# Kernel tuning notes

Hardware: AMD Instinct MI355X
Metric: run time of the kernel (lower is better)

The kernel has to match this reference:

```python
import jax, jax.numpy as jnp
import numpy as np

B, DIM, H = 65536, 1024, 16
HD = DIM // H  # head dim = 64


def setup_inputs() -> dict:
    key = jax.random.key(0)
    ks = jax.random.split(key, 6)
    x = jax.random.normal(ks[0], (B, DIM), dtype=jnp.float32)
    y = jax.random.normal(ks[1], (B, DIM), dtype=jnp.float32)
    mask = jnp.zeros((B,), dtype=jnp.bool_)  # unused by the module
    # Parameters (qkv_bias=False -> no bias on q/kv; proj has bias)
    Wq = jax.random.normal(ks[2], (DIM, DIM), dtype=jnp.float32) * 0.02
    Wkv = jax.random.normal(ks[3], (DIM, 2 * DIM), dtype=jnp.float32) * 0.02
    Wproj = jax.random.normal(ks[4], (DIM, DIM), dtype=jnp.float32) * 0.02
    bproj = jax.random.normal(ks[5], (DIM,), dtype=jnp.float32) * 0.02
    return {"x": x, "y": y, "mask": mask, "Wq": Wq, "Wkv": Wkv,
            "Wproj": Wproj, "bproj": bproj}


def reference(x, y, mask, Wq, Wkv, Wproj, bproj):
    # mask is accepted but unused, matching the original module.
    scale = HD ** (-0.5)
    q = x @ Wq                      # [B, DIM]
    kv = y @ Wkv                    # [B, 2*DIM]
    k, v = jnp.split(kv, 2, axis=-1)
    # b (h d) -> b h d
    q = q.reshape(B, H, HD) * scale  # first scale (q *= scale)
    k = k.reshape(B, H, HD)
    v = v.reshape(B, H, HD)
    # per-head dot product, scaled AGAIN (faithful to original double-scale)
    dots = jnp.einsum("bhd,bhd->bh", q, k) * scale  # [B, H]
    attn = jax.nn.softmax(dots, axis=-1)             # softmax over heads
    out = attn[..., None] * v                        # [B, H, HD]
    out = out.reshape(B, DIM)                        # b h d -> b (h d)
    return out @ Wproj + bproj
```

## Files before the change

kernel.cpp:

```cpp
#include <hip/hip_runtime.h>

typedef unsigned short ushort_t;
typedef unsigned int   uint_t;

typedef ushort_t u16x8  __attribute__((ext_vector_type(8)));
typedef __bf16   bf16x8 __attribute__((ext_vector_type(8)));
typedef float    f32x4  __attribute__((ext_vector_type(4)));

#define DIMSZ 1024

__device__ __forceinline__ ushort_t f2bf(float f) {
  uint_t u = __builtin_bit_cast(uint_t, f);
  u += 0x7fffu + ((u >> 16) & 1u);
  return (ushort_t)(u >> 16);
}
__device__ __forceinline__ float bf2f(ushort_t h) {
  uint_t u = ((uint_t)h) << 16;
  return __builtin_bit_cast(float, u);
}
__device__ __forceinline__ void lds_load16(const void* g, void* l) {
  __builtin_amdgcn_global_load_lds((const __attribute__((address_space(1))) void*)g,
                                   (__attribute__((address_space(3))) void*)l, 16, 0, 0);
}
#define SCHED0() __builtin_amdgcn_sched_barrier(0)
#define WBAR() do { SCHED0(); __builtin_amdgcn_s_barrier(); SCHED0(); } while (0)

__global__ __launch_bounds__(256) void wtrans(const float* __restrict__ src, int ld,
                                              ushort_t* __restrict__ dst) {
  __shared__ ushort_t tile[32][33];
  const int bx = blockIdx.x, by = blockIdx.y;
  const int tx = threadIdx.x & 31, ty = threadIdx.x >> 5;
#pragma unroll
  for (int i = 0; i < 32; i += 8)
    tile[ty + i][tx] = f2bf(src[(size_t)(by * 32 + ty + i) * ld + bx * 32 + tx]);
  __syncthreads();
#pragma unroll
  for (int i = 0; i < 32; i += 8)
    dst[(size_t)(bx * 32 + ty + i) * 1024 + by * 32 + tx] = tile[tx][ty + i];
}

__global__ __launch_bounds__(256) void cvt_bf16(const float* __restrict__ s,
                                                ushort_t* __restrict__ d) {
  const size_t n8 = (size_t)65536 * 1024 / 8;
  const size_t stride = (size_t)gridDim.x * 256;
  for (size_t i = (size_t)blockIdx.x * 256 + threadIdx.x; i < n8; i += stride) {
    f32x4 f0 = *(const f32x4*)(s + i * 8);
    f32x4 f1 = *(const f32x4*)(s + i * 8 + 4);
    u16x8 o;
#pragma unroll
    for (int j = 0; j < 4; ++j) { o[j] = f2bf(f0[j]); o[4 + j] = f2bf(f1[j]); }
    *(u16x8*)(d + i * 8) = o;
  }
}

__global__ __launch_bounds__(256) void softmax16(float* __restrict__ d) {
  const int row = blockIdx.x * 256 + threadIdx.x;
  f32x4 v[4];
#pragma unroll
  for (int i = 0; i < 4; ++i) v[i] = *(const f32x4*)(d + (size_t)row * 16 + i * 4);
  float m = v[0][0];
#pragma unroll
  for (int i = 0; i < 4; ++i)
#pragma unroll
    for (int j = 0; j < 4; ++j) m = fmaxf(m, v[i][j]);
  float sum = 0.f;
#pragma unroll
  for (int i = 0; i < 4; ++i)
#pragma unroll
    for (int j = 0; j < 4; ++j) { v[i][j] = expf(v[i][j] - m); sum += v[i][j]; }
  const float r = 1.f / sum;
#pragma unroll
  for (int i = 0; i < 4; ++i) {
#pragma unroll
    for (int j = 0; j < 4; ++j) v[i][j] *= r;
    *(f32x4*)(d + (size_t)row * 16 + i * 4) = v[i];
  }
}

__global__ __launch_bounds__(256) void abk(const ushort_t* __restrict__ kvb,
                                           const float* __restrict__ at,
                                           ushort_t* __restrict__ ab) {
  const size_t stride = (size_t)gridDim.x * 256;
  for (size_t g = (size_t)blockIdx.x * 256 + threadIdx.x; g < (size_t)8388608; g += stride) {
    const int row = (int)(g >> 7), c8 = (int)(g & 127);
    const float sc = at[(size_t)row * 16 + (c8 >> 3)];
    u16x8 v8 = *(const u16x8*)(kvb + (size_t)row * 2048 + 1024 + c8 * 8);
    u16x8 o;
#pragma unroll
    for (int j = 0; j < 8; ++j) o[j] = f2bf(bf2f(v8[j]) * sc);
    *(u16x8*)(ab + (size_t)row * 1024 + c8 * 8) = o;
  }
}

template <int EPI>
__global__ __launch_bounds__(512, 2) void gemm8(const ushort_t* __restrict__ A,
                                                const ushort_t* __restrict__ Bt,
                                                void* __restrict__ Cv,
                                                const float* __restrict__ bias,
                                                const ushort_t* __restrict__ kvp,
                                                float* __restrict__ dots,
                                                int ldc, int ncol_lg2) {
  __shared__ ushort_t lds[65536];
  const int t = threadIdx.x;
  const int nb8 = gridDim.x >> 3;
  const int nbid = (blockIdx.x & 7) * nb8 + (blockIdx.x >> 3);
  const int n0 = (nbid & ((1 << ncol_lg2) - 1)) * 256;
  const int m0 = (nbid >> ncol_lg2) * 256;
  const int w = t >> 6, lane = t & 63;
  const int wm = w >> 2, wn = w & 3;
  const int lr = lane & 15, lk = lane >> 4;
  const int w512 = w * 512;

  const int srow = w * 8 + (lane >> 3);
  const int scsw = ((lane & 7) * 16) ^ ((srow & 7) << 4);
  const ushort_t* aS = A + (size_t)(m0 + srow) * DIMSZ + (scsw >> 1);
  const ushort_t* bS = Bt + (size_t)(n0 + srow) * DIMSZ + (scsw >> 1);

  const int cbe0 = (((lk * 16)) ^ ((lr & 7) << 4)) >> 1;
  const int cbe1 = ((64 + lk * 16) ^ ((lr & 7) << 4)) >> 1;
  const int aRB = lr * 64;
  const int bRB = 32768 + (wn * 64 + lr) * 64;

  f32x4 acc[8][4];
  const f32x4 zf = {0.f, 0.f, 0.f, 0.f};
#pragma unroll
  for (int i = 0; i < 8; ++i)
#pragma unroll
    for (int j = 0; j < 4; ++j) acc[i][j] = zf;
  bf16x8 a[4][2], b0[2][2], b1[2][2];

#define STAGE_A(cc, hh, tt) do {                                          \
    const ushort_t* s_ = aS + (size_t)(hh) * 65536 + (tt) * 64;           \
    ushort_t* d_ = lds + (cc) * 16384 + (hh) * 4096 + w512;               \
    lds_load16(s_, d_);                                                   \
    lds_load16(s_ + 131072, d_ + 8192); } while (0)
#define STAGE_B(cc, hh, tt) do {                                          \
    const ushort_t* s_ = bS + (size_t)(hh) * 131072 + (tt) * 64;          \
    ushort_t* d_ = lds + 32768 + (cc) * 16384 + (hh) * 8192 + w512;       \
    lds_load16(s_, d_);                                                   \
    lds_load16(s_ + 65536, d_ + 4096); } while (0)
#define LDA(cc, mq) do {                                                  \
    const ushort_t* Lp = lds + (cc) * 16384 + (wm * 2 + (mq)) * 4096 + aRB; \
    _Pragma("unroll") for (int j = 0; j < 4; ++j) {                       \
      a[j][0] = *(const bf16x8*)(Lp + j * 1024 + cbe0);                   \
      a[j][1] = *(const bf16x8*)(Lp + j * 1024 + cbe1); } } while (0)
#define LDB(cc, dst, nq) do {                                             \
    const ushort_t* Lp = lds + (cc) * 16384 + bRB + (nq) * 2048;          \
    _Pragma("unroll") for (int ni = 0; ni < 2; ++ni) {                    \
      dst[ni][0] = *(const bf16x8*)(Lp + ni * 1024 + cbe0);               \
      dst[ni][1] = *(const bf16x8*)(Lp + ni * 1024 + cbe1); } } while (0)
#define MMQ(mb, B, nb) do {                                               \
    _Pragma("unroll") for (int j = 0; j < 4; ++j)                         \
    _Pragma("unroll") for (int ni = 0; ni < 2; ++ni)                      \
    _Pragma("unroll") for (int ks = 0; ks < 2; ++ks)                      \
      acc[(mb) + j][(nb) + ni] = __builtin_amdgcn_mfma_f32_16x16x32_bf16( \
          a[j][ks], B[ni][ks], acc[(mb) + j][(nb) + ni], 0, 0, 0); } while (0)
#define TILE(S1, S2, VM, tv, c, nxt) do {                                 \
    LDA(c, 0); LDB(c, b0, 0);                                             \
    if (S1) STAGE_A(nxt, 1, (tv) + 1);                                    \
    WBAR();                                                               \
    __builtin_amdgcn_s_setprio(1); MMQ(0, b0, 0); __builtin_amdgcn_s_setprio(0); \
    WBAR();                                                               \
    LDB(c, b1, 1);                                                        \
    if (S2) STAGE_A(c, 0, (tv) + 2);                                      \
    WBAR();                                                               \
    __builtin_amdgcn_s_setprio(1); MMQ(0, b1, 2); __builtin_amdgcn_s_setprio(0); \
    WBAR();                                                               \
    LDA(c, 1);                                                            \
    if (S2) STAGE_B(c, 0, (tv) + 2);                                      \
    WBAR();                                                               \
    __builtin_amdgcn_s_setprio(1); MMQ(4, b1, 2); __builtin_amdgcn_s_setprio(0); \
    WBAR();                                                               \
    if (S2) STAGE_B(c, 1, (tv) + 2);                                      \
    if ((VM) == 6) { asm volatile("s_waitcnt vmcnt(6)" ::: "memory"); }   \
    else if ((VM) == 0) { asm volatile("s_waitcnt vmcnt(0)" ::: "memory"); } \
    WBAR();                                                               \
    __builtin_amdgcn_s_setprio(1); MMQ(4, b0, 0); __builtin_amdgcn_s_setprio(0); \
    WBAR();                                                               \
  } while (0)

  STAGE_A(0, 0, 0); STAGE_A(0, 1, 0); STAGE_B(0, 0, 0); STAGE_B(0, 1, 0);
  STAGE_A(1, 0, 1); STAGE_B(1, 0, 1); STAGE_B(1, 1, 1);
  asm volatile("s_waitcnt vmcnt(6)" ::: "memory");
  WBAR();

  for (int tt = 0; tt < 7; ++tt) {
    const int t0 = tt * 2;
    TILE(1, 1, 6, t0, 0, 1);
    TILE(1, 1, 6, t0 + 1, 1, 0);
  }
  TILE(1, 0, 0, 14, 0, 1);
  TILE(0, 0, -1, 15, 1, 0);

#undef TILE
#undef MMQ
#undef LDB
#undef LDA
#undef STAGE_B
#undef STAGE_A

  if constexpr (EPI == 0) {
    ushort_t* Cp = (ushort_t*)Cv;
    ushort_t* ep = lds + w * 8192;
#pragma unroll
    for (int mq = 0; mq < 2; ++mq)
#pragma unroll
      for (int j = 0; j < 4; ++j)
#pragma unroll
        for (int ni = 0; ni < 4; ++ni)
#pragma unroll
          for (int r = 0; r < 4; ++r) {
            const int row = mq * 64 + j * 16 + lk * 4 + r;
            const int ce = ((ni * 16 + lr) * 2) ^ ((row & 7) << 4);
            ep[row * 64 + (ce >> 1)] = f2bf(acc[mq * 4 + j][ni][r]);
          }
#pragma unroll
    for (int rr = 0; rr < 16; ++rr) {
      const int row = rr * 8 + (lane >> 3);
      const int ce = ((lane & 7) * 16) ^ ((lane >> 3) << 4);
      u16x8 vv = *(const u16x8*)(ep + row * 64 + (ce >> 1));
      *(u16x8*)(Cp + (size_t)(m0 + wm * 128 + row) * ldc + n0 + wn * 64 + (lane & 7) * 8) = vv;
    }
  } else if constexpr (EPI == 1) {
    float* Op = (float*)Cv;
    float bb[4];
#pragma unroll
    for (int ni = 0; ni < 4; ++ni) bb[ni] = bias[n0 + wn * 64 + ni * 16 + lr];
#pragma unroll
    for (int mq = 0; mq < 2; ++mq)
#pragma unroll
      for (int j = 0; j < 4; ++j)
#pragma unroll
        for (int ni = 0; ni < 4; ++ni)
#pragma unroll
          for (int r = 0; r < 4; ++r)
            Op[(size_t)(m0 + wm * 128 + mq * 64 + j * 16 + lk * 4 + r) * 1024 +
               n0 + wn * 64 + ni * 16 + lr] = acc[mq * 4 + j][ni][r] + bb[ni];
  } else {
    const int h = (n0 >> 6) + wn;
    ushort_t* kw = lds + w * 8192;
    const int rsub = lane >> 3, c8 = (lane & 7) * 8;
    const ushort_t* kS = kvp + (size_t)(m0 + wm * 128 + rsub) * 2048 + h * 64 + c8;
#pragma unroll
    for (int i = 0; i < 16; ++i)
      lds_load16(kS + (size_t)i * 8 * 2048, kw + i * 512);
    asm volatile("s_waitcnt vmcnt(0)" ::: "memory");
#pragma unroll
    for (int mq = 0; mq < 2; ++mq)
#pragma unroll
      for (int j = 0; j < 4; ++j)
#pragma unroll
        for (int r = 0; r < 4; ++r) {
          const int row = mq * 64 + j * 16 + lk * 4 + r;
          float p = 0.f;
#pragma unroll
          for (int ni = 0; ni < 4; ++ni)
            p += acc[mq * 4 + j][ni][r] * bf2f(kw[row * 64 + ni * 16 + lr]);
#pragma unroll
          for (int off = 1; off < 16; off <<= 1) p += __shfl_xor(p, off, 16);
          if (lr == 0)
            dots[(size_t)(m0 + wm * 128 + row) * 16 + h] = p * 0.015625f;
        }
  }
}

extern "C" void kernel_launch(void* const* d_in, const int* in_sizes, int n_in,
                              void* d_out, int out_size, void* d_ws, size_t ws_size,
                              hipStream_t stream) {
  const float* x   = (const float*)d_in[0];
  const float* y   = (const float*)d_in[1];
  const float* Wq  = (const float*)d_in[3];
  const float* Wkv = (const float*)d_in[4];
  const float* Wp  = (const float*)d_in[5];
  const float* bp  = (const float*)d_in[6];
  (void)in_sizes; (void)n_in; (void)out_size; (void)ws_size;

  char* ws = (char*)d_ws;
  ushort_t* Wqt   = (ushort_t*)(ws);
  ushort_t* Wkvt  = (ushort_t*)(ws + (2ull   << 20));
  ushort_t* Wpt   = (ushort_t*)(ws + (6ull   << 20));
  float*    dotsb = (float*)   (ws + (8ull   << 20));
  ushort_t* kvb   = (ushort_t*)(ws + (12ull  << 20));
  ushort_t* actb  = (ushort_t*)(ws + (268ull << 20));

  wtrans<<<dim3(32, 32), 256, 0, stream>>>(Wq, 1024, Wqt);
  wtrans<<<dim3(64, 32), 256, 0, stream>>>(Wkv, 2048, Wkvt);
  wtrans<<<dim3(32, 32), 256, 0, stream>>>(Wp, 1024, Wpt);

  cvt_bf16<<<4096, 256, 0, stream>>>(y, actb);
  gemm8<0><<<2048, 512, 0, stream>>>(actb, Wkvt, kvb, nullptr, nullptr, nullptr, 2048, 3);

  cvt_bf16<<<4096, 256, 0, stream>>>(x, actb);
  gemm8<2><<<1024, 512, 0, stream>>>(actb, Wqt, nullptr, nullptr, kvb, dotsb, 1024, 2);

  softmax16<<<256, 256, 0, stream>>>(dotsb);

  abk<<<2048, 256, 0, stream>>>(kvb, dotsb, actb);

  gemm8<1><<<1024, 512, 0, stream>>>(actb, Wpt, d_out, bp, nullptr, nullptr, 1024, 2);
}
```

Before: 813.6 us.

## Simplify GEMM main loop to whole-tile double buffering with fewer barriers

Replaces the fine-grained 8-wave ping-pong schedule, which staged quarter tiles between MMA phases and had eight barriers per tile, with a simpler loop. Each iteration now loads all B fragments and the A fragments, runs all MFMAs, then issues the full next-next tile load behind a single barrier pair. The LDS layout becomes two contiguous 256x64 A|B buffers. This cuts barrier and scheduling overhead but gives up the fine interleaving of global-to-LDS loads with compute, and keeps more B fragments live in registers.

```diff
diff --git a/kernel.cpp b/kernel.cpp
--- a/kernel.cpp
+++ b/kernel.cpp
@@ -109,17 +109,16 @@
   const int w = t >> 6, lane = t & 63;
   const int wm = w >> 2, wn = w & 3;
   const int lr = lane & 15, lk = lane >> 4;
-  const int w512 = w * 512;
-
-  const int srow = w * 8 + (lane >> 3);
-  const int scsw = ((lane & 7) * 16) ^ ((srow & 7) << 4);
-  const ushort_t* aS = A + (size_t)(m0 + srow) * DIMSZ + (scsw >> 1);
-  const ushort_t* bS = Bt + (size_t)(n0 + srow) * DIMSZ + (scsw >> 1);
-
-  const int cbe0 = (((lk * 16)) ^ ((lr & 7) << 4)) >> 1;
+
+  const int sr = lane >> 3;
+  const int scsw = ((lane & 7) * 16) ^ ((sr & 7) << 4);
+  const ushort_t* aS = A + (size_t)(m0 + w * 8 + sr) * DIMSZ + (scsw >> 1);
+  const ushort_t* bS = Bt + (size_t)(n0 + w * 8 + sr) * DIMSZ + (scsw >> 1);
+
+  const int cbe0 = ((lk * 16) ^ ((lr & 7) << 4)) >> 1;
   const int cbe1 = ((64 + lk * 16) ^ ((lr & 7) << 4)) >> 1;
-  const int aRB = lr * 64;
-  const int bRB = 32768 + (wn * 64 + lr) * 64;
+  const int aRowB = (wm * 128 + lr) * 64;
+  const int bRowB = 16384 + (wn * 64 + lr) * 64;
 
   f32x4 acc[8][4];
   const f32x4 zf = {0.f, 0.f, 0.f, 0.f};
@@ -127,77 +126,62 @@
   for (int i = 0; i < 8; ++i)
 #pragma unroll
     for (int j = 0; j < 4; ++j) acc[i][j] = zf;
-  bf16x8 a[4][2], b0[2][2], b1[2][2];
-
-#define STAGE_A(cc, hh, tt) do {                                          \
-    const ushort_t* s_ = aS + (size_t)(hh) * 65536 + (tt) * 64;           \
-    ushort_t* d_ = lds + (cc) * 16384 + (hh) * 4096 + w512;               \
-    lds_load16(s_, d_);                                                   \
-    lds_load16(s_ + 131072, d_ + 8192); } while (0)
-#define STAGE_B(cc, hh, tt) do {                                          \
-    const ushort_t* s_ = bS + (size_t)(hh) * 131072 + (tt) * 64;          \
-    ushort_t* d_ = lds + 32768 + (cc) * 16384 + (hh) * 8192 + w512;       \
-    lds_load16(s_, d_);                                                   \
-    lds_load16(s_ + 65536, d_ + 4096); } while (0)
-#define LDA(cc, mq) do {                                                  \
-    const ushort_t* Lp = lds + (cc) * 16384 + (wm * 2 + (mq)) * 4096 + aRB; \
-    _Pragma("unroll") for (int j = 0; j < 4; ++j) {                       \
-      a[j][0] = *(const bf16x8*)(Lp + j * 1024 + cbe0);                   \
+  bf16x8 a[4][2], b[4][2];
+
+#define STG(cc, tt) do {                                                    \
+    _Pragma("unroll") for (int i_ = 0; i_ < 4; ++i_)                        \
+      lds_load16(aS + (size_t)i_ * 64 * DIMSZ + (tt) * 64,                  \
+                 lds + (cc) * 32768 + (i_ * 64 + w * 8) * 64);              \
+    _Pragma("unroll") for (int i_ = 0; i_ < 4; ++i_)                        \
+      lds_load16(bS + (size_t)i_ * 64 * DIMSZ + (tt) * 64,                  \
+                 lds + (cc) * 32768 + 16384 + (i_ * 64 + w * 8) * 64);      \
+  } while (0)
+#define LDA4(cc, mq) do {                                                   \
+    const ushort_t* Lp = lds + (cc) * 32768 + aRowB + (mq) * 4096;          \
+    _Pragma("unroll") for (int j = 0; j < 4; ++j) {                         \
+      a[j][0] = *(const bf16x8*)(Lp + j * 1024 + cbe0);                     \
       a[j][1] = *(const bf16x8*)(Lp + j * 1024 + cbe1); } } while (0)
-#define LDB(cc, dst, nq) do {                                             \
-    const ushort_t* Lp = lds + (cc) * 16384 + bRB + (nq) * 2048;          \
-    _Pragma("unroll") for (int ni = 0; ni < 2; ++ni) {                    \
-      dst[ni][0] = *(const bf16x8*)(Lp + ni * 1024 + cbe0);               \
-      dst[ni][1] = *(const bf16x8*)(Lp + ni * 1024 + cbe1); } } while (0)
-#define MMQ(mb, B, nb) do {                                               \
-    _Pragma("unroll") for (int j = 0; j < 4; ++j)                         \
-    _Pragma("unroll") for (int ni = 0; ni < 2; ++ni)                      \
-    _Pragma("unroll") for (int ks = 0; ks < 2; ++ks)                      \
-      acc[(mb) + j][(nb) + ni] = __builtin_amdgcn_mfma_f32_16x16x32_bf16( \
-          a[j][ks], B[ni][ks], acc[(mb) + j][(nb) + ni], 0, 0, 0); } while (0)
-#define TILE(S1, S2, VM, tv, c, nxt) do {                                 \
-    LDA(c, 0); LDB(c, b0, 0);                                             \
-    if (S1) STAGE_A(nxt, 1, (tv) + 1);                                    \
-    WBAR();                                                               \
-    __builtin_amdgcn_s_setprio(1); MMQ(0, b0, 0); __builtin_amdgcn_s_setprio(0); \
-    WBAR();                                                               \
-    LDB(c, b1, 1);                                                        \
-    if (S2) STAGE_A(c, 0, (tv) + 2);                                      \
-    WBAR();                                                               \
-    __builtin_amdgcn_s_setprio(1); MMQ(0, b1, 2); __builtin_amdgcn_s_setprio(0); \
-    WBAR();                                                               \
-    LDA(c, 1);                                                            \
-    if (S2) STAGE_B(c, 0, (tv) + 2);                                      \
-    WBAR();                                                               \
-    __builtin_amdgcn_s_setprio(1); MMQ(4, b1, 2); __builtin_amdgcn_s_setprio(0); \
-    WBAR();                                                               \
-    if (S2) STAGE_B(c, 1, (tv) + 2);                                      \
-    if ((VM) == 6) { asm volatile("s_waitcnt vmcnt(6)" ::: "memory"); }   \
-    else if ((VM) == 0) { asm volatile("s_waitcnt vmcnt(0)" ::: "memory"); } \
-    WBAR();                                                               \
-    __builtin_amdgcn_s_setprio(1); MMQ(4, b0, 0); __builtin_amdgcn_s_setprio(0); \
-    WBAR();                                                               \
+#define LDB4(cc) do {                                                       \
+    const ushort_t* Lp = lds + (cc) * 32768 + bRowB;                        \
+    _Pragma("unroll") for (int ni = 0; ni < 4; ++ni) {                      \
+      b[ni][0] = *(const bf16x8*)(Lp + ni * 1024 + cbe0);                   \
+      b[ni][1] = *(const bf16x8*)(Lp + ni * 1024 + cbe1); } } while (0)
+#define MMQ(mb) do {                                                        \
+    _Pragma("unroll") for (int j = 0; j < 4; ++j)                           \
+    _Pragma("unroll") for (int ni = 0; ni < 4; ++ni)                        \
+    _Pragma("unroll") for (int ks = 0; ks < 2; ++ks)                        \
+      acc[(mb) + j][ni] = __builtin_amdgcn_mfma_f32_16x16x32_bf16(          \
+          a[j][ks], b[ni][ks], acc[(mb) + j][ni], 0, 0, 0); } while (0)
+#define TILE(S, VM, tv, cc) do {                                            \
+    LDB4(cc);                                                               \
+    LDA4(cc, 0);                                                            \
+    __builtin_amdgcn_s_setprio(1); MMQ(0); __builtin_amdgcn_s_setprio(0);   \
+    LDA4(cc, 1);                                                            \
+    __builtin_amdgcn_s_setprio(1); MMQ(4); __builtin_amdgcn_s_setprio(0);   \
+    WBAR();                                                                 \
+    if (S) STG(cc, (tv) + 2);                                               \
+    if ((VM) == 8)      asm volatile("s_waitcnt vmcnt(8)" ::: "memory");    \
+    else if ((VM) == 0) asm volatile("s_waitcnt vmcnt(0)" ::: "memory");    \
+    WBAR();                                                                 \
   } while (0)
 
-  STAGE_A(0, 0, 0); STAGE_A(0, 1, 0); STAGE_B(0, 0, 0); STAGE_B(0, 1, 0);
-  STAGE_A(1, 0, 1); STAGE_B(1, 0, 1); STAGE_B(1, 1, 1);
-  asm volatile("s_waitcnt vmcnt(6)" ::: "memory");
+  STG(0, 0); STG(1, 1);
+  asm volatile("s_waitcnt vmcnt(8)" ::: "memory");
   WBAR();
 
   for (int tt = 0; tt < 7; ++tt) {
     const int t0 = tt * 2;
-    TILE(1, 1, 6, t0, 0, 1);
-    TILE(1, 1, 6, t0 + 1, 1, 0);
-  }
-  TILE(1, 0, 0, 14, 0, 1);
-  TILE(0, 0, -1, 15, 1, 0);
+    TILE(1, 8, t0, 0);
+    TILE(1, 8, t0 + 1, 1);
+  }
+  TILE(0, 0, 14, 0);
+  TILE(0, -1, 15, 1);
 
 #undef TILE
 #undef MMQ
-#undef LDB
-#undef LDA
-#undef STAGE_B
-#undef STAGE_A
+#undef LDB4
+#undef LDA4
+#undef STG
 
   if constexpr (EPI == 0) {
     ushort_t* Cp = (ushort_t*)Cv;
```

Measured after the change: 882.2 us. +8.4%, slower.

## Split KV GEMM and fuse attention scaling into V GEMM epilogue

Applied to the files above, without the earlier changes.

Computes K and V with separate GEMMs, deferring the V projection until after softmax so its epilogue multiplies each row-head by the attention weight and writes bf16 directly. This removes the standalone abk kernel and the write/read of the full KV buffer. Weight transposes are merged into a single launch writing a concatenated transposed weight buffer. Buffers are reused (x bf16 buffer overwritten by scaled V), which adds ordering dependence.

```diff
diff --git a/kernel.cpp b/kernel.cpp
--- a/kernel.cpp
+++ b/kernel.cpp
@@ -25,18 +25,25 @@
 #define SCHED0() __builtin_amdgcn_sched_barrier(0)
 #define WBAR() do { SCHED0(); __builtin_amdgcn_s_barrier(); SCHED0(); } while (0)
 
-__global__ __launch_bounds__(256) void wtrans(const float* __restrict__ src, int ld,
-                                              ushort_t* __restrict__ dst) {
+__global__ __launch_bounds__(256) void wtrans4(const float* __restrict__ Wq,
+                                               const float* __restrict__ Wkv,
+                                               const float* __restrict__ Wp,
+                                               ushort_t* __restrict__ dst) {
   __shared__ ushort_t tile[32][33];
   const int bx = blockIdx.x, by = blockIdx.y;
+  const int n0 = bx * 32;
+  const float* src; int ld, c0;
+  if (n0 < 1024)      { src = Wq;  ld = 1024; c0 = n0; }
+  else if (n0 < 3072) { src = Wkv; ld = 2048; c0 = n0 - 1024; }
+  else                { src = Wp;  ld = 1024; c0 = n0 - 3072; }
   const int tx = threadIdx.x & 31, ty = threadIdx.x >> 5;
 #pragma unroll
   for (int i = 0; i < 32; i += 8)
-    tile[ty + i][tx] = f2bf(src[(size_t)(by * 32 + ty + i) * ld + bx * 32 + tx]);
+    tile[ty + i][tx] = f2bf(src[(size_t)(by * 32 + ty + i) * ld + c0 + tx]);
   __syncthreads();
 #pragma unroll
   for (int i = 0; i < 32; i += 8)
-    dst[(size_t)(bx * 32 + ty + i) * 1024 + by * 32 + tx] = tile[tx][ty + i];
+    dst[(size_t)(n0 + ty + i) * 1024 + by * 32 + tx] = tile[tx][ty + i];
 }
 
 __global__ __launch_bounds__(256) void cvt_bf16(const float* __restrict__ s,
@@ -74,21 +81,6 @@
 #pragma unroll
     for (int j = 0; j < 4; ++j) v[i][j] *= r;
     *(f32x4*)(d + (size_t)row * 16 + i * 4) = v[i];
-  }
-}
-
-__global__ __launch_bounds__(256) void abk(const ushort_t* __restrict__ kvb,
-                                           const float* __restrict__ at,
-                                           ushort_t* __restrict__ ab) {
-  const size_t stride = (size_t)gridDim.x * 256;
-  for (size_t g = (size_t)blockIdx.x * 256 + threadIdx.x; g < (size_t)8388608; g += stride) {
-    const int row = (int)(g >> 7), c8 = (int)(g & 127);
-    const float sc = at[(size_t)row * 16 + (c8 >> 3)];
-    u16x8 v8 = *(const u16x8*)(kvb + (size_t)row * 2048 + 1024 + c8 * 8);
-    u16x8 o;
-#pragma unroll
-    for (int j = 0; j < 8; ++j) o[j] = f2bf(bf2f(v8[j]) * sc);
-    *(u16x8*)(ab + (size_t)row * 1024 + c8 * 8) = o;
   }
 }
 
@@ -199,21 +191,26 @@
 #undef STAGE_B
 #undef STAGE_A
 
-  if constexpr (EPI == 0) {
+  if constexpr (EPI == 0 || EPI == 3) {
     ushort_t* Cp = (ushort_t*)Cv;
     ushort_t* ep = lds + w * 8192;
+    const int h = (n0 >> 6) + wn;
 #pragma unroll
     for (int mq = 0; mq < 2; ++mq)
 #pragma unroll
       for (int j = 0; j < 4; ++j)
 #pragma unroll
-        for (int ni = 0; ni < 4; ++ni)
-#pragma unroll
-          for (int r = 0; r < 4; ++r) {
-            const int row = mq * 64 + j * 16 + lk * 4 + r;
+        for (int r = 0; r < 4; ++r) {
+          const int row = mq * 64 + j * 16 + lk * 4 + r;
+          float sc = 1.f;
+          if (EPI == 3)
+            sc = bias[(size_t)(m0 + wm * 128 + row) * 16 + h];
+#pragma unroll
+          for (int ni = 0; ni < 4; ++ni) {
             const int ce = ((ni * 16 + lr) * 2) ^ ((row & 7) << 4);
-            ep[row * 64 + (ce >> 1)] = f2bf(acc[mq * 4 + j][ni][r]);
+            ep[row * 64 + (ce >> 1)] = f2bf(acc[mq * 4 + j][ni][r] * sc);
           }
+        }
 #pragma unroll
     for (int rr = 0; rr < 16; ++rr) {
       const int row = rr * 8 + (lane >> 3);
@@ -240,10 +237,10 @@
     const int h = (n0 >> 6) + wn;
     ushort_t* kw = lds + w * 8192;
     const int rsub = lane >> 3, c8 = (lane & 7) * 8;
-    const ushort_t* kS = kvp + (size_t)(m0 + wm * 128 + rsub) * 2048 + h * 64 + c8;
+    const ushort_t* kS = kvp + (size_t)(m0 + wm * 128 + rsub) * 1024 + h * 64 + c8;
 #pragma unroll
     for (int i = 0; i < 16; ++i)
-      lds_load16(kS + (size_t)i * 8 * 2048, kw + i * 512);
+      lds_load16(kS + (size_t)i * 8 * 1024, kw + i * 512);
     asm volatile("s_waitcnt vmcnt(0)" ::: "memory");
 #pragma unroll
     for (int mq = 0; mq < 2; ++mq)
@@ -276,26 +273,28 @@
   (void)in_sizes; (void)n_in; (void)out_size; (void)ws_size;
 
   char* ws = (char*)d_ws;
-  ushort_t* Wqt   = (ushort_t*)(ws);
-  ushort_t* Wkvt  = (ushort_t*)(ws + (2ull   << 20));
-  ushort_t* Wpt   = (ushort_t*)(ws + (6ull   << 20));
+  ushort_t* Wall  = (ushort_t*)(ws);
   float*    dotsb = (float*)   (ws + (8ull   << 20));
-  ushort_t* kvb   = (ushort_t*)(ws + (12ull  << 20));
-  ushort_t* actb  = (ushort_t*)(ws + (268ull << 20));
-
-  wtrans<<<dim3(32, 32), 256, 0, stream>>>(Wq, 1024, Wqt);
-  wtrans<<<dim3(64, 32), 256, 0, stream>>>(Wkv, 2048, Wkvt);
-  wtrans<<<dim3(32, 32), 256, 0, stream>>>(Wp, 1024, Wpt);
-
-  cvt_bf16<<<4096, 256, 0, stream>>>(y, actb);
-  gemm8<0><<<2048, 512, 0, stream>>>(actb, Wkvt, kvb, nullptr, nullptr, nullptr, 2048, 3);
-
-  cvt_bf16<<<4096, 256, 0, stream>>>(x, actb);
-  gemm8<2><<<1024, 512, 0, stream>>>(actb, Wqt, nullptr, nullptr, kvb, dotsb, 1024, 2);
+  ushort_t* yb    = (ushort_t*)(ws + (12ull  << 20));
+  ushort_t* xb    = (ushort_t*)(ws + (140ull << 20));
+  ushort_t* kb    = (ushort_t*)(ws + (268ull << 20));
+
+  const ushort_t* Wqt = Wall;
+  const ushort_t* Wkt = Wall + (size_t)1024 * 1024;
+  const ushort_t* Wvt = Wall + (size_t)2048 * 1024;
+  const ushort_t* Wpt = Wall + (size_t)3072 * 1024;
+
+  wtrans4<<<dim3(128, 32), 256, 0, stream>>>(Wq, Wkv, Wp, Wall);
+
+  cvt_bf16<<<4096, 256, 0, stream>>>(y, yb);
+  gemm8<0><<<1024, 512, 0, stream>>>(yb, Wkt, kb, nullptr, nullptr, nullptr, 1024, 2);
+
+  cvt_bf16<<<4096, 256, 0, stream>>>(x, xb);
+  gemm8<2><<<1024, 512, 0, stream>>>(xb, Wqt, nullptr, nullptr, kb, dotsb, 1024, 2);
 
   softmax16<<<256, 256, 0, stream>>>(dotsb);
 
-  abk<<<2048, 256, 0, stream>>>(kvb, dotsb, actb);
-
-  gemm8<1><<<1024, 512, 0, stream>>>(actb, Wpt, d_out, bp, nullptr, nullptr, 1024, 2);
-}
+  gemm8<3><<<1024, 512, 0, stream>>>(yb, Wvt, xb, dotsb, nullptr, nullptr, 1024, 2);
+
+  gemm8<1><<<1024, 512, 0, stream>>>(xb, Wpt, d_out, bp, nullptr, nullptr, 1024, 2);
+}
```

Result: faster. 757.8 us (-6.9%).
